# Optimization experiments

Measured on AMD Instinct MI355X. Metric: run time of the kernel, lower is better.

Reference implementation:

```python
import jax, jax.numpy as jnp
import numpy as np

HEADS = 8

def _conv1x1(x, W, b):
    # x: [n, Cin, H, W]; W: [Cout, Cin]; b: [Cout]
    return jnp.einsum('nchw,oc->nohw', x, W) + b[None, :, None, None]

def setup_inputs() -> dict:
    key = jax.random.key(0)
    ks = jax.random.split(key, 11)
    n, Cin, H, W = 8, 256, 80, 80
    Ck, Cv = 256, 256
    s_in = 1.0 / np.sqrt(Cin)
    s_v = 1.0 / np.sqrt(Cv)
    return {
        'query_feature': jax.random.normal(ks[0], (n, Cin, H, W), jnp.float32),
        'key_feature': jax.random.normal(ks[1], (n, Cin, H, W), jnp.float32),
        'value_feature': jax.random.normal(ks[2], (n, Cin, H, W), jnp.float32),
        'Wq': jax.random.normal(ks[3], (Ck, Cin), jnp.float32) * s_in,
        'bq': jax.random.normal(ks[4], (Ck,), jnp.float32) * s_in,
        'Wk': jax.random.normal(ks[5], (Ck, Cin), jnp.float32) * s_in,
        'bk': jax.random.normal(ks[6], (Ck,), jnp.float32) * s_in,
        'Wv': jax.random.normal(ks[7], (Cv, Cin), jnp.float32) * s_in,
        'bv': jax.random.normal(ks[8], (Cv,), jnp.float32) * s_in,
        'Wr': jax.random.normal(ks[9], (Cin, Cv), jnp.float32) * s_v,
        'br': jax.random.normal(ks[10], (Cin,), jnp.float32) * s_v,
    }

def reference(query_feature, key_feature, value_feature, Wq, bq, Wk, bk, Wv, bv, Wr, br):
    n, _, qh, qw = query_feature.shape
    kvn, _, kvh, kvw = key_feature.shape
    Ck = Wq.shape[0]
    Cv = Wv.shape[0]
    hk = Ck // HEADS
    hv = Cv // HEADS
    Lq = qh * qw
    Lkv = kvh * kvw
    # 1x1 conv projections, split channels into heads (consecutive channel blocks)
    q = _conv1x1(query_feature, Wq, bq).reshape(n, HEADS, hk, Lq)
    k = _conv1x1(key_feature, Wk, bk).reshape(kvn, HEADS, hk, Lkv)
    v = _conv1x1(value_feature, Wv, bv).reshape(kvn, HEADS, hv, Lkv)
    # softmax: keys over spatial positions, queries over head channels
    k = jax.nn.softmax(k, axis=3)
    q = jax.nn.softmax(q, axis=2)
    # efficient (linear) attention: context = K @ V^T, out = context^T @ Q
    context = jnp.einsum('nhkl,nhvl->nhkv', k, v)          # [n, H, hk, hv]
    attended = jnp.einsum('nhkv,nhkl->nhvl', context, q)   # [n, H, hv, Lq]
    aggregated = attended.reshape(n, Cv, qh, qw)
    return _conv1x1(aggregated, Wr, br) + query_feature
```

## Files before the change

### kernel.cpp

```cpp
#include <hip/hip_runtime.h>
#include <hip/hip_bf16.h>

#define NB 8
#define C 256
#define LL 6400
#define HEADS 8
#define HC 32
#define NH 64
#define CH 40
#define CHUNK 160
#define KCHUNKS 25

typedef unsigned short u16;
typedef unsigned int u32;
typedef __attribute__((ext_vector_type(8))) short bf16x8;
typedef __attribute__((ext_vector_type(4))) float f32x4;

typedef __attribute__((address_space(1))) const u32 ga_u32;
typedef __attribute__((address_space(3))) u32 ls_u32;

__device__ __forceinline__ void gload_lds16(const u16* g, u16* l) {
  __builtin_amdgcn_global_load_lds((ga_u32*)g, (ls_u32*)l, 16, 0, 0);
}

__device__ __forceinline__ float bf2f(u32 u) { return __uint_as_float(u << 16); }
__device__ __forceinline__ u16 f2bf(float f) {
  __hip_bfloat16 h = __float2bfloat16(f);
  return *(u16*)&h;
}
__device__ __forceinline__ void unpack8(uint4 u, float* f) {
  f[0] = bf2f(u.x & 0xffffu); f[1] = bf2f(u.x >> 16);
  f[2] = bf2f(u.y & 0xffffu); f[3] = bf2f(u.y >> 16);
  f[4] = bf2f(u.z & 0xffffu); f[5] = bf2f(u.z >> 16);
  f[6] = bf2f(u.w & 0xffffu); f[7] = bf2f(u.w >> 16);
}

__global__ __launch_bounds__(256) void transpose_cvt(const float* __restrict__ X,
                                                     u16* __restrict__ Xt) {
  __shared__ float tl[64][65];
  const int n = blockIdx.z, l0 = blockIdx.x * 64, c0 = blockIdx.y * 64;
  const int t = threadIdx.x;
  const int rr = t >> 4;
  const int lc = (t & 15) * 4;
  const float* Xn = X + (size_t)n * C * LL;
#pragma unroll
  for (int p = 0; p < 4; ++p) {
    const int row = p * 16 + rr;
    float4 v = *(const float4*)&Xn[(size_t)(c0 + row) * LL + l0 + lc];
    tl[row][lc + 0] = v.x; tl[row][lc + 1] = v.y;
    tl[row][lc + 2] = v.z; tl[row][lc + 3] = v.w;
  }
  __syncthreads();
  u16* XtN = Xt + (size_t)n * LL * C;
  const int cc = (t & 15) * 4;
#pragma unroll
  for (int p = 0; p < 4; ++p) {
    const int lrow = p * 16 + rr;
    ushort4 o;
    o.x = f2bf(tl[cc + 0][lrow]); o.y = f2bf(tl[cc + 1][lrow]);
    o.z = f2bf(tl[cc + 2][lrow]); o.w = f2bf(tl[cc + 3][lrow]);
    *(ushort4*)&XtN[(size_t)(l0 + lrow) * C + c0 + cc] = o;
  }
}

__global__ __launch_bounds__(256) void cvt_bf16(const float* __restrict__ src,
                                                u16* __restrict__ dst) {
  const int i = (blockIdx.x * 256 + threadIdx.x) * 4;
  float4 v = *(const float4*)&src[i];
  ushort4 o = {f2bf(v.x), f2bf(v.y), f2bf(v.z), f2bf(v.w)};
  *(ushort4*)&dst[i] = o;
}

__global__ __launch_bounds__(256) void proj_mfma(const u16* __restrict__ Xt,
    const u16* __restrict__ Wb, const float* __restrict__ bias,
    u16* __restrict__ Pt) {
  __shared__ __align__(16) u16 As[4096];
  __shared__ __align__(16) u16 Bs[4096];
  const int n = blockIdx.z;
  const int l0 = blockIdx.x * 128;
  const int co0 = blockIdx.y * 128;
  const int t = threadIdx.x;
  const int lane = t & 63, wave = t >> 6;
  const int wm = (wave >> 1) * 64, wn = (wave & 1) * 64;
  const int srow = t >> 2;
  const int scol = (t & 3) * 8;
  const u16* XtN = Xt + (size_t)n * LL * C;
  f32x4 acc[4][4] = {};
  for (int k0 = 0; k0 < C; k0 += 32) {
    __syncthreads();
    gload_lds16(&XtN[(size_t)(l0 + srow) * C + k0 + scol], &As[wave * 512]);
    gload_lds16(&XtN[(size_t)(l0 + 64 + srow) * C + k0 + scol], &As[2048 + wave * 512]);
    gload_lds16(&Wb[(size_t)(co0 + srow) * C + k0 + scol], &Bs[wave * 512]);
    gload_lds16(&Wb[(size_t)(co0 + 64 + srow) * C + k0 + scol], &Bs[2048 + wave * 512]);
    __syncthreads();
    const int fr = lane & 15, quad = lane >> 4;
    bf16x8 a[4], b[4];
#pragma unroll
    for (int i = 0; i < 4; ++i)
      a[i] = *(const bf16x8*)&As[(wm + i * 16 + fr) * 32 + quad * 8];
#pragma unroll
    for (int j = 0; j < 4; ++j)
      b[j] = *(const bf16x8*)&Bs[(wn + j * 16 + fr) * 32 + quad * 8];
#pragma unroll
    for (int i = 0; i < 4; ++i)
#pragma unroll
      for (int j = 0; j < 4; ++j)
        acc[i][j] = __builtin_amdgcn_mfma_f32_16x16x32_bf16(a[i], b[j], acc[i][j], 0, 0, 0);
  }
  u16* PtN = Pt + (size_t)n * LL * C;
  const int fr = lane & 15, quad = lane >> 4;
  const int colc = co0 + wn + fr;
  float bv[4];
#pragma unroll
  for (int j = 0; j < 4; ++j) bv[j] = bias[colc + j * 16];
#pragma unroll
  for (int i = 0; i < 4; ++i) {
    const int lrow = l0 + wm + i * 16 + quad * 4;
#pragma unroll
    for (int r = 0; r < 4; ++r)
#pragma unroll
      for (int j = 0; j < 4; ++j)
        PtN[(size_t)(lrow + r) * C + colc + j * 16] = f2bf(acc[i][j][r] + bv[j]);
  }
}

__global__ __launch_bounds__(256) void kstats(const u16* __restrict__ Kt,
    float* __restrict__ pmax, float* __restrict__ psum) {
  const int chk = blockIdx.x, n = blockIdx.y;
  const int t = threadIdx.x;
  const int c2 = t & 127, ph = t >> 7;
  const u16* base = Kt + ((size_t)n * LL + chk * 256) * C + c2 * 2;
  float m0 = -1e30f, m1 = -1e30f;
  for (int i = 0; i < 128; ++i) {
    u32 u = *(const u32*)&base[(size_t)(2 * i + ph) * C];
    m0 = fmaxf(m0, bf2f(u & 0xffffu)); m1 = fmaxf(m1, bf2f(u >> 16));
  }
  __shared__ float sm[2][256];
  sm[ph][c2 * 2] = m0; sm[ph][c2 * 2 + 1] = m1;
  __syncthreads();
  m0 = fmaxf(sm[0][c2 * 2], sm[1][c2 * 2]);
  m1 = fmaxf(sm[0][c2 * 2 + 1], sm[1][c2 * 2 + 1]);
  float s0 = 0.f, s1 = 0.f;
  for (int i = 0; i < 128; ++i) {
    u32 u = *(const u32*)&base[(size_t)(2 * i + ph) * C];
    s0 += __expf(bf2f(u & 0xffffu) - m0);
    s1 += __expf(bf2f(u >> 16) - m1);
  }
  __syncthreads();
  sm[ph][c2 * 2] = s0; sm[ph][c2 * 2 + 1] = s1;
  __syncthreads();
  if (ph == 0) {
    const int idx = (n * KCHUNKS + chk) * 256 + c2 * 2;
    pmax[idx] = m0; pmax[idx + 1] = m1;
    psum[idx] = sm[0][c2 * 2] + sm[1][c2 * 2];
    psum[idx + 1] = sm[0][c2 * 2 + 1] + sm[1][c2 * 2 + 1];
  }
}

__global__ __launch_bounds__(256) void kmerge(const float* __restrict__ pmax,
    const float* __restrict__ psum, float* __restrict__ kmax, float* __restrict__ krs) {
  const int n = blockIdx.x, c = threadIdx.x;
  float m = -1e30f;
  for (int ch = 0; ch < KCHUNKS; ++ch)
    m = fmaxf(m, pmax[(n * KCHUNKS + ch) * 256 + c]);
  float s = 0.f;
  for (int ch = 0; ch < KCHUNKS; ++ch)
    s += psum[(n * KCHUNKS + ch) * 256 + c] * __expf(pmax[(n * KCHUNKS + ch) * 256 + c] - m);
  kmax[n * 256 + c] = m;
  krs[n * 256 + c] = 1.0f / s;
}

__global__ __launch_bounds__(256) void qsoftmax(u16* __restrict__ Qt) {
  const int t = threadIdx.x;
  const int lane = t & 63, wave = t >> 6;
  const int g = lane >> 2, sub = lane & 3;
  const int gid = (blockIdx.x * 4 + wave) * 16 + g;
  const int h = gid & 7;
  const size_t row = (size_t)(gid >> 3);
  u16* p = Qt + row * C + h * 32 + sub * 8;
  uint4 u = *(const uint4*)p;
  float v[8]; unpack8(u, v);
  float m = v[0];
#pragma unroll
  for (int j = 1; j < 8; ++j) m = fmaxf(m, v[j]);
  m = fmaxf(m, __shfl_xor(m, 1));
  m = fmaxf(m, __shfl_xor(m, 2));
  float e[8], s = 0.f;
#pragma unroll
  for (int j = 0; j < 8; ++j) { e[j] = __expf(v[j] - m); s += e[j]; }
  s += __shfl_xor(s, 1);
  s += __shfl_xor(s, 2);
  const float r = 1.0f / s;
  union { uint4 u; u16 h[8]; } o;
#pragma unroll
  for (int j = 0; j < 8; ++j) o.h[j] = f2bf(e[j] * r);
  *(uint4*)p = o.u;
}

__global__ __launch_bounds__(64) void ctx_partial(const u16* __restrict__ Kt,
    const u16* __restrict__ Vt, const float* __restrict__ kmax,
    const float* __restrict__ krs, float* __restrict__ part) {
  __shared__ float Ks[32][36];
  __shared__ float Vs[32][36];
  const int nh = blockIdx.y, chk = blockIdx.x;
  const int n = nh >> 3, h = nh & 7;
  const int lane = threadIdx.x;
  const int rr = lane >> 2, koff = (lane & 3) * 8;
  float km[8];
#pragma unroll
  for (int j = 0; j < 8; ++j) km[j] = kmax[n * C + h * 32 + koff + j];
  const size_t rowbase = ((size_t)n * LL + chk * CHUNK) * C + h * 32 + koff;
  const int k4 = (lane & 7) * 4, v4 = (lane >> 3) * 4;
  float acc[4][4];
#pragma unroll
  for (int i = 0; i < 4; ++i)
#pragma unroll
    for (int j = 0; j < 4; ++j) acc[i][j] = 0.f;
  for (int ls = 0; ls < CHUNK; ls += 32) {
    __syncthreads();
#pragma unroll
    for (int p = 0; p < 2; ++p) {
      const int r = p * 16 + rr;
      uint4 ku = *(const uint4*)&Kt[rowbase + (size_t)(ls + r) * C];
      uint4 vu = *(const uint4*)&Vt[rowbase + (size_t)(ls + r) * C];
      float kf[8], vf[8];
      unpack8(ku, kf); unpack8(vu, vf);
#pragma unroll
      for (int j = 0; j < 8; ++j) {
        Ks[r][koff + j] = __expf(kf[j] - km[j]);
        Vs[r][koff + j] = vf[j];
      }
    }
    __syncthreads();
#pragma unroll
    for (int l = 0; l < 32; ++l) {
      float a[4], b[4];
      *(float4*)a = *(const float4*)&Ks[l][k4];
      *(float4*)b = *(const float4*)&Vs[l][v4];
#pragma unroll
      for (int i = 0; i < 4; ++i)
#pragma unroll
        for (int j = 0; j < 4; ++j) acc[i][j] = fmaf(a[i], b[j], acc[i][j]);
    }
  }
#pragma unroll
  for (int i = 0; i < 4; ++i) {
    const float rs = krs[n * C + h * 32 + k4 + i];
#pragma unroll
    for (int j = 0; j < 4; ++j)
      part[(((size_t)chk * NH + nh) * HC + k4 + i) * HC + v4 + j] = acc[i][j] * rs;
  }
}

__global__ __launch_bounds__(256) void ctx_reduce(const float* __restrict__ part,
                                                  float* __restrict__ ctx) {
  const int idx = blockIdx.x * 256 + threadIdx.x;
  float s = 0.f;
  for (int c = 0; c < CH; ++c) s += part[(size_t)c * (NH * HC * HC) + idx];
  ctx[idx] = s;
}

__global__ __launch_bounds__(256) void mfuse(const float* __restrict__ Wr,
    const float* __restrict__ ctx, u16* __restrict__ M) {
  const int idx = blockIdx.x * 256 + threadIdx.x;
  const int hk = idx & 255;
  const int o = (idx >> 8) & 255;
  const int n = idx >> 16;
  const int h = hk >> 5, k = hk & 31;
  const float* wr = Wr + (size_t)o * C + h * HC;
  const float* cx = ctx + ((size_t)(n * HEADS + h) * HC + k) * HC;
  float s = 0.f;
#pragma unroll
  for (int v = 0; v < HC; ++v) s = fmaf(wr[v], cx[v], s);
  M[idx] = f2bf(s);
}

__global__ __launch_bounds__(256) void out_mfma(const u16* __restrict__ Qt,
    const u16* __restrict__ Mb, const float* __restrict__ br,
    const float* __restrict__ Xq, float* __restrict__ out) {
  __shared__ __align__(16) u16 As[4096];
  __shared__ __align__(16) u16 Bs[4096];
  const int n = blockIdx.z;
  const int l0 = blockIdx.x * 128;
  const int co0 = blockIdx.y * 128;
  const int t = threadIdx.x;
  const int lane = t & 63, wave = t >> 6;
  const int wm = (wave >> 1) * 64, wn = (wave & 1) * 64;
  const int srow = t >> 2;
  const int scol = (t & 3) * 8;
  const u16* MbN = Mb + (size_t)n * C * C;
  const u16* QtN = Qt + (size_t)n * LL * C;
  f32x4 acc[4][4] = {};
  for (int k0 = 0; k0 < C; k0 += 32) {
    __syncthreads();
    gload_lds16(&MbN[(size_t)(co0 + srow) * C + k0 + scol], &As[wave * 512]);
    gload_lds16(&MbN[(size_t)(co0 + 64 + srow) * C + k0 + scol], &As[2048 + wave * 512]);
    gload_lds16(&QtN[(size_t)(l0 + srow) * C + k0 + scol], &Bs[wave * 512]);
    gload_lds16(&QtN[(size_t)(l0 + 64 + srow) * C + k0 + scol], &Bs[2048 + wave * 512]);
    __syncthreads();
    const int fr = lane & 15, quad = lane >> 4;
    bf16x8 a[4], b[4];
#pragma unroll
    for (int i = 0; i < 4; ++i)
      a[i] = *(const bf16x8*)&As[(wm + i * 16 + fr) * 32 + quad * 8];
#pragma unroll
    for (int j = 0; j < 4; ++j)
      b[j] = *(const bf16x8*)&Bs[(wn + j * 16 + fr) * 32 + quad * 8];
#pragma unroll
    for (int i = 0; i < 4; ++i)
#pragma unroll
      for (int j = 0; j < 4; ++j)
        acc[i][j] = __builtin_amdgcn_mfma_f32_16x16x32_bf16(a[i], b[j], acc[i][j], 0, 0, 0);
  }
  const float* XqN = Xq + (size_t)n * C * LL;
  float* On = out + (size_t)n * C * LL;
  const int fr = lane & 15, quad = lane >> 4;
#pragma unroll
  for (int i = 0; i < 4; ++i) {
#pragma unroll
    for (int r = 0; r < 4; ++r) {
      const int co = co0 + wm + i * 16 + quad * 4 + r;
      const float bb = br[co];
#pragma unroll
      for (int j = 0; j < 4; ++j) {
        const int l = l0 + wn + j * 16 + fr;
        const size_t off = (size_t)co * LL + l;
        On[off] = acc[i][j][r] + bb + XqN[off];
      }
    }
  }
}

extern "C" void kernel_launch(void* const* d_in, const int* in_sizes, int n_in,
                              void* d_out, int out_size, void* d_ws, size_t ws_size,
                              hipStream_t stream) {
  const float* Xq = (const float*)d_in[0];
  const float* Xk = (const float*)d_in[1];
  const float* Xv = (const float*)d_in[2];
  const float* Wq = (const float*)d_in[3];
  const float* bq = (const float*)d_in[4];
  const float* Wk = (const float*)d_in[5];
  const float* bk = (const float*)d_in[6];
  const float* Wv = (const float*)d_in[7];
  const float* bv = (const float*)d_in[8];
  const float* Wr = (const float*)d_in[9];
  const float* br = (const float*)d_in[10];
  float* out = (float*)d_out;

  char* ws = (char*)d_ws;
  const size_t nelem = (size_t)NB * LL * C;
  u16* Xt = (u16*)ws;
  u16* Qt = (u16*)(ws + nelem * 2);
  u16* Kt = (u16*)(ws + nelem * 4);
  u16* Vt = (u16*)(ws + nelem * 6);
  char* p = ws + nelem * 8;
  u16* Wqb = (u16*)p; p += C * C * 2;
  u16* Wkb = (u16*)p; p += C * C * 2;
  u16* Wvb = (u16*)p; p += C * C * 2;
  u16* Mb = (u16*)p;  p += (size_t)NB * C * C * 2;
  float* pmax = (float*)p; p += KCHUNKS * NB * C * 4;
  float* psum = (float*)p; p += KCHUNKS * NB * C * 4;
  float* kmax = (float*)p; p += NB * C * 4;
  float* krs = (float*)p;  p += NB * C * 4;
  float* ctx = (float*)p;  p += NH * HC * HC * 4;
  float* part = (float*)p;

  const dim3 gT(100, 4, NB);
  const dim3 gG(50, 2, NB);

  cvt_bf16<<<64, 256, 0, stream>>>(Wq, Wqb);
  cvt_bf16<<<64, 256, 0, stream>>>(Wk, Wkb);
  cvt_bf16<<<64, 256, 0, stream>>>(Wv, Wvb);

  transpose_cvt<<<gT, 256, 0, stream>>>(Xq, Xt);
  proj_mfma<<<gG, 256, 0, stream>>>(Xt, Wqb, bq, Qt);
  transpose_cvt<<<gT, 256, 0, stream>>>(Xk, Xt);
  proj_mfma<<<gG, 256, 0, stream>>>(Xt, Wkb, bk, Kt);
  transpose_cvt<<<gT, 256, 0, stream>>>(Xv, Xt);
  proj_mfma<<<gG, 256, 0, stream>>>(Xt, Wvb, bv, Vt);

  qsoftmax<<<NB * LL * HEADS / 64, 256, 0, stream>>>(Qt);
  kstats<<<dim3(KCHUNKS, NB), 256, 0, stream>>>(Kt, pmax, psum);
  kmerge<<<NB, 256, 0, stream>>>(pmax, psum, kmax, krs);
  ctx_partial<<<dim3(CH, NH), 64, 0, stream>>>(Kt, Vt, kmax, krs, part);
  ctx_reduce<<<NH * HC * HC / 256, 256, 0, stream>>>(part, ctx);
  mfuse<<<NB * C * C / 256, 256, 0, stream>>>(Wr, ctx, Mb);
  out_mfma<<<gG, 256, 0, stream>>>(Qt, Mb, br, Xq, out);
}
```

Measured before the change: 359.1 us.

## Fuse transpose into projections, drop K max pass, fuse Q softmax into output GEMM

Projections now read fp32 NCHW input directly, converting and transposing into LDS inside a single batched launch for Q, K and V. This removes the bf16 transposed staging buffer and its extra pass. The key softmax no longer computes a running max: exp(k) is accumulated along with its row sums, and normalisation happens in ctx_reduce. The query softmax is computed per tile inside the output GEMM. Removing the max subtraction risks overflow for large key logits.

```diff
diff --git a/kernel.cpp b/kernel.cpp
--- a/kernel.cpp
+++ b/kernel.cpp
@@ -7,9 +7,10 @@
 #define HEADS 8
 #define HC 32
 #define NH 64
-#define CH 40
-#define CHUNK 160
-#define KCHUNKS 25
+#define SEG 40
+#define SL 160
+#define ATP 40
+#define QPP 264
 
 typedef unsigned short u16;
 typedef unsigned int u32;
@@ -35,229 +36,152 @@
   f[6] = bf2f(u.w & 0xffffu); f[7] = bf2f(u.w >> 16);
 }
 
-__global__ __launch_bounds__(256) void transpose_cvt(const float* __restrict__ X,
-                                                     u16* __restrict__ Xt) {
-  __shared__ float tl[64][65];
-  const int n = blockIdx.z, l0 = blockIdx.x * 64, c0 = blockIdx.y * 64;
-  const int t = threadIdx.x;
-  const int rr = t >> 4;
-  const int lc = (t & 15) * 4;
-  const float* Xn = X + (size_t)n * C * LL;
-#pragma unroll
-  for (int p = 0; p < 4; ++p) {
-    const int row = p * 16 + rr;
-    float4 v = *(const float4*)&Xn[(size_t)(c0 + row) * LL + l0 + lc];
-    tl[row][lc + 0] = v.x; tl[row][lc + 1] = v.y;
-    tl[row][lc + 2] = v.z; tl[row][lc + 3] = v.w;
-  }
-  __syncthreads();
-  u16* XtN = Xt + (size_t)n * LL * C;
-  const int cc = (t & 15) * 4;
-#pragma unroll
-  for (int p = 0; p < 4; ++p) {
-    const int lrow = p * 16 + rr;
-    ushort4 o;
-    o.x = f2bf(tl[cc + 0][lrow]); o.y = f2bf(tl[cc + 1][lrow]);
-    o.z = f2bf(tl[cc + 2][lrow]); o.w = f2bf(tl[cc + 3][lrow]);
-    *(ushort4*)&XtN[(size_t)(l0 + lrow) * C + c0 + cc] = o;
-  }
-}
-
-__global__ __launch_bounds__(256) void cvt_bf16(const float* __restrict__ src,
-                                                u16* __restrict__ dst) {
-  const int i = (blockIdx.x * 256 + threadIdx.x) * 4;
-  float4 v = *(const float4*)&src[i];
+struct WcvtArgs { const float* W[3]; u16* Wb[3]; };
+struct PFArgs { const float* X[3]; const u16* Wb[3]; const float* bias[3]; u16* P[3]; };
+
+__global__ __launch_bounds__(256) void wcvt(WcvtArgs a) {
+  const int idx = blockIdx.x * 256 + threadIdx.x;
+  const int which = idx >> 14, off = (idx & 16383) * 4;
+  float4 v = *(const float4*)&a.W[which][off];
   ushort4 o = {f2bf(v.x), f2bf(v.y), f2bf(v.z), f2bf(v.w)};
-  *(ushort4*)&dst[i] = o;
-}
-
-__global__ __launch_bounds__(256) void proj_mfma(const u16* __restrict__ Xt,
-    const u16* __restrict__ Wb, const float* __restrict__ bias,
-    u16* __restrict__ Pt) {
-  __shared__ __align__(16) u16 As[4096];
-  __shared__ __align__(16) u16 Bs[4096];
-  const int n = blockIdx.z;
+  *(ushort4*)&a.Wb[which][off] = o;
+}
+
+__global__ __launch_bounds__(256, 2) void proj_fused(PFArgs args) {
+  __shared__ __align__(16) u16 At[128 * ATP];
+  __shared__ __align__(16) u16 Bs[256 * 32];
+  const int which = blockIdx.y >> 3, n = blockIdx.y & 7;
   const int l0 = blockIdx.x * 128;
-  const int co0 = blockIdx.y * 128;
   const int t = threadIdx.x;
   const int lane = t & 63, wave = t >> 6;
-  const int wm = (wave >> 1) * 64, wn = (wave & 1) * 64;
-  const int srow = t >> 2;
-  const int scol = (t & 3) * 8;
-  const u16* XtN = Xt + (size_t)n * LL * C;
-  f32x4 acc[4][4] = {};
+  const int fr = lane & 15, q = lane >> 4;
+  const int wl = (wave >> 1) * 64, wco = (wave & 1) * 128;
+  const int s32 = t & 31, rcg = t >> 5;
+  const int srow = t >> 2, scol = (t & 3) * 8;
+  const float* X = args.X[which] + (size_t)n * C * LL;
+  const u16* Wb = args.Wb[which];
+  f32x4 acc[4][8] = {};
+  float4 xv[4];
+#pragma unroll
+  for (int j = 0; j < 4; ++j)
+    xv[j] = *(const float4*)&X[(size_t)(rcg * 4 + j) * LL + l0 + s32 * 4];
   for (int k0 = 0; k0 < C; k0 += 32) {
     __syncthreads();
-    gload_lds16(&XtN[(size_t)(l0 + srow) * C + k0 + scol], &As[wave * 512]);
-    gload_lds16(&XtN[(size_t)(l0 + 64 + srow) * C + k0 + scol], &As[2048 + wave * 512]);
-    gload_lds16(&Wb[(size_t)(co0 + srow) * C + k0 + scol], &Bs[wave * 512]);
-    gload_lds16(&Wb[(size_t)(co0 + 64 + srow) * C + k0 + scol], &Bs[2048 + wave * 512]);
+#pragma unroll
+    for (int s = 0; s < 4; ++s)
+      gload_lds16(&Wb[(size_t)(s * 64 + srow) * C + k0 + scol],
+                  &Bs[s * 2048 + wave * 512]);
+    const float* xf = (const float*)xv;
+#pragma unroll
+    for (int li = 0; li < 4; ++li) {
+      const int lp = li ^ (s32 & 3);
+      u32 lo = (u32)f2bf(xf[0 * 4 + lp]) | ((u32)f2bf(xf[1 * 4 + lp]) << 16);
+      u32 hi = (u32)f2bf(xf[2 * 4 + lp]) | ((u32)f2bf(xf[3 * 4 + lp]) << 16);
+      u32* dst = (u32*)&At[(s32 * 4 + lp) * ATP + rcg * 4];
+      dst[0] = lo; dst[1] = hi;
+    }
     __syncthreads();
-    const int fr = lane & 15, quad = lane >> 4;
-    bf16x8 a[4], b[4];
+    if (k0 + 32 < C) {
+#pragma unroll
+      for (int j = 0; j < 4; ++j)
+        xv[j] = *(const float4*)&X[(size_t)(k0 + 32 + rcg * 4 + j) * LL + l0 + s32 * 4];
+    }
+    bf16x8 a[4];
 #pragma unroll
     for (int i = 0; i < 4; ++i)
-      a[i] = *(const bf16x8*)&As[(wm + i * 16 + fr) * 32 + quad * 8];
-#pragma unroll
-    for (int j = 0; j < 4; ++j)
-      b[j] = *(const bf16x8*)&Bs[(wn + j * 16 + fr) * 32 + quad * 8];
+      a[i] = *(const bf16x8*)&At[(wl + i * 16 + fr) * ATP + q * 8];
+#pragma unroll
+    for (int j = 0; j < 8; ++j) {
+      bf16x8 b = *(const bf16x8*)&Bs[(wco + j * 16 + fr) * 32 + q * 8];
+#pragma unroll
+      for (int i = 0; i < 4; ++i)
+        acc[i][j] = __builtin_amdgcn_mfma_f32_16x16x32_bf16(a[i], b, acc[i][j], 0, 0, 0);
+    }
+  }
+  const float* bias = args.bias[which];
+  u16* P = args.P[which] + (size_t)n * LL * C;
+  float bb[8];
+#pragma unroll
+  for (int j = 0; j < 8; ++j) bb[j] = bias[wco + j * 16 + fr];
+#pragma unroll
+  for (int i = 0; i < 4; ++i)
+#pragma unroll
+    for (int r = 0; r < 4; ++r) {
+      const int lrow = l0 + wl + i * 16 + q * 4 + r;
+#pragma unroll
+      for (int j = 0; j < 8; ++j)
+        P[(size_t)lrow * C + wco + j * 16 + fr] = f2bf(acc[i][j][r] + bb[j]);
+    }
+}
+
+__global__ __launch_bounds__(256) void ctx_part(const u16* __restrict__ Kt,
+    const u16* __restrict__ Vt, float* __restrict__ pctx, float* __restrict__ psum) {
+  __shared__ __align__(16) u16 Ks[16 * 256];
+  __shared__ __align__(16) u16 Vs[16 * 256];
+  const int seg = blockIdx.x, n = blockIdx.y;
+  const int t = threadIdx.x, lane = t & 63, wave = t >> 6;
+  const int l0 = seg * SL;
+  const u16* KtN = Kt + (size_t)n * LL * C;
+  const u16* VtN = Vt + (size_t)n * LL * C;
+  const int k4 = (lane & 7) * 4, v8 = lane >> 3;
+  float acc[2][4][4] = {};
+  float ssum[2][4] = {};
+  for (int ls = 0; ls < SL; ls += 16) {
+    __syncthreads();
+#pragma unroll
+    for (int i = 0; i < 2; ++i) {
+      const int r = wave * 4 + i * 2;
+      gload_lds16(&KtN[(size_t)(l0 + ls + r) * C + lane * 8], &Ks[r * 256]);
+      gload_lds16(&VtN[(size_t)(l0 + ls + r) * C + lane * 8], &Vs[r * 256]);
+    }
+    __syncthreads();
+#pragma unroll
+    for (int hh = 0; hh < 2; ++hh) {
+      const int h = wave * 2 + hh;
+#pragma unroll
+      for (int l = 0; l < 16; ++l) {
+        ushort4 ku = *(const ushort4*)&Ks[l * 256 + h * 32 + k4];
+        ushort4 vu = *(const ushort4*)&Vs[l * 256 + h * 32 + v8 * 4];
+        float ek[4] = {__expf(bf2f(ku.x)), __expf(bf2f(ku.y)),
+                       __expf(bf2f(ku.z)), __expf(bf2f(ku.w))};
+        float vf[4] = {bf2f(vu.x), bf2f(vu.y), bf2f(vu.z), bf2f(vu.w)};
+#pragma unroll
+        for (int i = 0; i < 4; ++i)
+#pragma unroll
+          for (int j = 0; j < 4; ++j) acc[hh][i][j] = fmaf(ek[i], vf[j], acc[hh][i][j]);
+        if (v8 == 0)
+#pragma unroll
+          for (int i = 0; i < 4; ++i) ssum[hh][i] += ek[i];
+      }
+    }
+  }
+#pragma unroll
+  for (int hh = 0; hh < 2; ++hh) {
+    const int h = wave * 2 + hh;
+    const size_t pb = ((size_t)seg * NH + n * 8 + h) * 1024;
 #pragma unroll
     for (int i = 0; i < 4; ++i)
 #pragma unroll
       for (int j = 0; j < 4; ++j)
-        acc[i][j] = __builtin_amdgcn_mfma_f32_16x16x32_bf16(a[i], b[j], acc[i][j], 0, 0, 0);
-  }
-  u16* PtN = Pt + (size_t)n * LL * C;
-  const int fr = lane & 15, quad = lane >> 4;
-  const int colc = co0 + wn + fr;
-  float bv[4];
-#pragma unroll
-  for (int j = 0; j < 4; ++j) bv[j] = bias[colc + j * 16];
-#pragma unroll
-  for (int i = 0; i < 4; ++i) {
-    const int lrow = l0 + wm + i * 16 + quad * 4;
-#pragma unroll
-    for (int r = 0; r < 4; ++r)
-#pragma unroll
-      for (int j = 0; j < 4; ++j)
-        PtN[(size_t)(lrow + r) * C + colc + j * 16] = f2bf(acc[i][j][r] + bv[j]);
-  }
-}
-
-__global__ __launch_bounds__(256) void kstats(const u16* __restrict__ Kt,
-    float* __restrict__ pmax, float* __restrict__ psum) {
-  const int chk = blockIdx.x, n = blockIdx.y;
-  const int t = threadIdx.x;
-  const int c2 = t & 127, ph = t >> 7;
-  const u16* base = Kt + ((size_t)n * LL + chk * 256) * C + c2 * 2;
-  float m0 = -1e30f, m1 = -1e30f;
-  for (int i = 0; i < 128; ++i) {
-    u32 u = *(const u32*)&base[(size_t)(2 * i + ph) * C];
-    m0 = fmaxf(m0, bf2f(u & 0xffffu)); m1 = fmaxf(m1, bf2f(u >> 16));
-  }
-  __shared__ float sm[2][256];
-  sm[ph][c2 * 2] = m0; sm[ph][c2 * 2 + 1] = m1;
-  __syncthreads();
-  m0 = fmaxf(sm[0][c2 * 2], sm[1][c2 * 2]);
-  m1 = fmaxf(sm[0][c2 * 2 + 1], sm[1][c2 * 2 + 1]);
-  float s0 = 0.f, s1 = 0.f;
-  for (int i = 0; i < 128; ++i) {
-    u32 u = *(const u32*)&base[(size_t)(2 * i + ph) * C];
-    s0 += __expf(bf2f(u & 0xffffu) - m0);
-    s1 += __expf(bf2f(u >> 16) - m1);
-  }
-  __syncthreads();
-  sm[ph][c2 * 2] = s0; sm[ph][c2 * 2 + 1] = s1;
-  __syncthreads();
-  if (ph == 0) {
-    const int idx = (n * KCHUNKS + chk) * 256 + c2 * 2;
-    pmax[idx] = m0; pmax[idx + 1] = m1;
-    psum[idx] = sm[0][c2 * 2] + sm[1][c2 * 2];
-    psum[idx + 1] = sm[0][c2 * 2 + 1] + sm[1][c2 * 2 + 1];
-  }
-}
-
-__global__ __launch_bounds__(256) void kmerge(const float* __restrict__ pmax,
-    const float* __restrict__ psum, float* __restrict__ kmax, float* __restrict__ krs) {
-  const int n = blockIdx.x, c = threadIdx.x;
-  float m = -1e30f;
-  for (int ch = 0; ch < KCHUNKS; ++ch)
-    m = fmaxf(m, pmax[(n * KCHUNKS + ch) * 256 + c]);
-  float s = 0.f;
-  for (int ch = 0; ch < KCHUNKS; ++ch)
-    s += psum[(n * KCHUNKS + ch) * 256 + c] * __expf(pmax[(n * KCHUNKS + ch) * 256 + c] - m);
-  kmax[n * 256 + c] = m;
-  krs[n * 256 + c] = 1.0f / s;
-}
-
-__global__ __launch_bounds__(256) void qsoftmax(u16* __restrict__ Qt) {
-  const int t = threadIdx.x;
-  const int lane = t & 63, wave = t >> 6;
-  const int g = lane >> 2, sub = lane & 3;
-  const int gid = (blockIdx.x * 4 + wave) * 16 + g;
-  const int h = gid & 7;
-  const size_t row = (size_t)(gid >> 3);
-  u16* p = Qt + row * C + h * 32 + sub * 8;
-  uint4 u = *(const uint4*)p;
-  float v[8]; unpack8(u, v);
-  float m = v[0];
-#pragma unroll
-  for (int j = 1; j < 8; ++j) m = fmaxf(m, v[j]);
-  m = fmaxf(m, __shfl_xor(m, 1));
-  m = fmaxf(m, __shfl_xor(m, 2));
-  float e[8], s = 0.f;
-#pragma unroll
-  for (int j = 0; j < 8; ++j) { e[j] = __expf(v[j] - m); s += e[j]; }
-  s += __shfl_xor(s, 1);
-  s += __shfl_xor(s, 2);
-  const float r = 1.0f / s;
-  union { uint4 u; u16 h[8]; } o;
-#pragma unroll
-  for (int j = 0; j < 8; ++j) o.h[j] = f2bf(e[j] * r);
-  *(uint4*)p = o.u;
-}
-
-__global__ __launch_bounds__(64) void ctx_partial(const u16* __restrict__ Kt,
-    const u16* __restrict__ Vt, const float* __restrict__ kmax,
-    const float* __restrict__ krs, float* __restrict__ part) {
-  __shared__ float Ks[32][36];
-  __shared__ float Vs[32][36];
-  const int nh = blockIdx.y, chk = blockIdx.x;
-  const int n = nh >> 3, h = nh & 7;
-  const int lane = threadIdx.x;
-  const int rr = lane >> 2, koff = (lane & 3) * 8;
-  float km[8];
-#pragma unroll
-  for (int j = 0; j < 8; ++j) km[j] = kmax[n * C + h * 32 + koff + j];
-  const size_t rowbase = ((size_t)n * LL + chk * CHUNK) * C + h * 32 + koff;
-  const int k4 = (lane & 7) * 4, v4 = (lane >> 3) * 4;
-  float acc[4][4];
-#pragma unroll
-  for (int i = 0; i < 4; ++i)
-#pragma unroll
-    for (int j = 0; j < 4; ++j) acc[i][j] = 0.f;
-  for (int ls = 0; ls < CHUNK; ls += 32) {
-    __syncthreads();
-#pragma unroll
-    for (int p = 0; p < 2; ++p) {
-      const int r = p * 16 + rr;
-      uint4 ku = *(const uint4*)&Kt[rowbase + (size_t)(ls + r) * C];
-      uint4 vu = *(const uint4*)&Vt[rowbase + (size_t)(ls + r) * C];
-      float kf[8], vf[8];
-      unpack8(ku, kf); unpack8(vu, vf);
-#pragma unroll
-      for (int j = 0; j < 8; ++j) {
-        Ks[r][koff + j] = __expf(kf[j] - km[j]);
-        Vs[r][koff + j] = vf[j];
-      }
-    }
-    __syncthreads();
-#pragma unroll
-    for (int l = 0; l < 32; ++l) {
-      float a[4], b[4];
-      *(float4*)a = *(const float4*)&Ks[l][k4];
-      *(float4*)b = *(const float4*)&Vs[l][v4];
-#pragma unroll
-      for (int i = 0; i < 4; ++i)
-#pragma unroll
-        for (int j = 0; j < 4; ++j) acc[i][j] = fmaf(a[i], b[j], acc[i][j]);
-    }
-  }
-#pragma unroll
-  for (int i = 0; i < 4; ++i) {
-    const float rs = krs[n * C + h * 32 + k4 + i];
-#pragma unroll
-    for (int j = 0; j < 4; ++j)
-      part[(((size_t)chk * NH + nh) * HC + k4 + i) * HC + v4 + j] = acc[i][j] * rs;
-  }
-}
-
-__global__ __launch_bounds__(256) void ctx_reduce(const float* __restrict__ part,
-                                                  float* __restrict__ ctx) {
+        pctx[pb + (size_t)(k4 + i) * 32 + v8 * 4 + j] = acc[hh][i][j];
+    if (v8 == 0) {
+      const size_t sb = ((size_t)seg * NH + n * 8 + h) * 32;
+#pragma unroll
+      for (int i = 0; i < 4; ++i) psum[sb + k4 + i] = ssum[hh][i];
+    }
+  }
+}
+
+__global__ __launch_bounds__(256) void ctx_reduce(const float* __restrict__ pctx,
+    const float* __restrict__ psum, float* __restrict__ ctx) {
   const int idx = blockIdx.x * 256 + threadIdx.x;
-  float s = 0.f;
-  for (int c = 0; c < CH; ++c) s += part[(size_t)c * (NH * HC * HC) + idx];
-  ctx[idx] = s;
+  const int nh = idx >> 10, e = idx & 1023, k = e >> 5;
+  float s = 0.f, ss = 0.f;
+  for (int g = 0; g < SEG; ++g) {
+    s += pctx[(size_t)(g * NH + nh) * 1024 + e];
+    ss += psum[(size_t)(g * NH + nh) * 32 + k];
+  }
+  ctx[idx] = s / ss;
 }
 
 __global__ __launch_bounds__(256) void mfuse(const float* __restrict__ Wr,
@@ -275,60 +199,78 @@
   M[idx] = f2bf(s);
 }
 
-__global__ __launch_bounds__(256) void out_mfma(const u16* __restrict__ Qt,
+__global__ __launch_bounds__(256) void out_fused(const u16* __restrict__ Qt,
     const u16* __restrict__ Mb, const float* __restrict__ br,
     const float* __restrict__ Xq, float* __restrict__ out) {
-  __shared__ __align__(16) u16 As[4096];
-  __shared__ __align__(16) u16 Bs[4096];
-  const int n = blockIdx.z;
-  const int l0 = blockIdx.x * 128;
-  const int co0 = blockIdx.y * 128;
-  const int t = threadIdx.x;
-  const int lane = t & 63, wave = t >> 6;
-  const int wm = (wave >> 1) * 64, wn = (wave & 1) * 64;
-  const int srow = t >> 2;
-  const int scol = (t & 3) * 8;
+  __shared__ __align__(16) u16 Qp[64 * QPP];
+  __shared__ __align__(16) u16 As[128 * 32];
+  const int n = blockIdx.y, l0 = blockIdx.x * 64;
+  const int t = threadIdx.x, lane = t & 63, wave = t >> 6;
+  const int fr = lane & 15, q = lane >> 4;
+  const int wcoL = (wave >> 1) * 64, wl = (wave & 1) * 32;
+  const u16* QtN = Qt + (size_t)n * LL * C;
+#pragma unroll
+  for (int p = 0; p < 2; ++p) {
+    const int row = p * 32 + (t >> 3);
+    const int g = t & 7;
+    const uint4* src = (const uint4*)&QtN[(size_t)(l0 + row) * C + g * 32];
+    uint4 u0 = src[0], u1 = src[1], u2 = src[2], u3 = src[3];
+    float v[32];
+    unpack8(u0, v); unpack8(u1, v + 8); unpack8(u2, v + 16); unpack8(u3, v + 24);
+    float e[32], s = 0.f;
+#pragma unroll
+    for (int j = 0; j < 32; ++j) { e[j] = __expf(v[j]); s += e[j]; }
+    const float r = 1.0f / s;
+    uint4* drow = (uint4*)&Qp[row * QPP + g * 32];
+#pragma unroll
+    for (int b4 = 0; b4 < 4; ++b4) {
+      union { uint4 u; u16 h[8]; } o;
+#pragma unroll
+      for (int j = 0; j < 8; ++j) o.h[j] = f2bf(e[b4 * 8 + j] * r);
+      drow[b4] = o.u;
+    }
+  }
+  f32x4 acc[2][4][2] = {};
   const u16* MbN = Mb + (size_t)n * C * C;
-  const u16* QtN = Qt + (size_t)n * LL * C;
-  f32x4 acc[4][4] = {};
-  for (int k0 = 0; k0 < C; k0 += 32) {
-    __syncthreads();
-    gload_lds16(&MbN[(size_t)(co0 + srow) * C + k0 + scol], &As[wave * 512]);
-    gload_lds16(&MbN[(size_t)(co0 + 64 + srow) * C + k0 + scol], &As[2048 + wave * 512]);
-    gload_lds16(&QtN[(size_t)(l0 + srow) * C + k0 + scol], &Bs[wave * 512]);
-    gload_lds16(&QtN[(size_t)(l0 + 64 + srow) * C + k0 + scol], &Bs[2048 + wave * 512]);
-    __syncthreads();
-    const int fr = lane & 15, quad = lane >> 4;
-    bf16x8 a[4], b[4];
-#pragma unroll
-    for (int i = 0; i < 4; ++i)
-      a[i] = *(const bf16x8*)&As[(wm + i * 16 + fr) * 32 + quad * 8];
-#pragma unroll
-    for (int j = 0; j < 4; ++j)
-      b[j] = *(const bf16x8*)&Bs[(wn + j * 16 + fr) * 32 + quad * 8];
-#pragma unroll
-    for (int i = 0; i < 4; ++i)
-#pragma unroll
-      for (int j = 0; j < 4; ++j)
-        acc[i][j] = __builtin_amdgcn_mfma_f32_16x16x32_bf16(a[i], b[j], acc[i][j], 0, 0, 0);
-  }
+  const int srow = t >> 2, scol = (t & 3) * 8;
+  for (int coh = 0; coh < 2; ++coh)
+    for (int k0 = 0; k0 < C; k0 += 32) {
+      __syncthreads();
+#pragma unroll
+      for (int s = 0; s < 2; ++s)
+        gload_lds16(&MbN[(size_t)(coh * 128 + s * 64 + srow) * C + k0 + scol],
+                    &As[s * 2048 + wave * 512]);
+      __syncthreads();
+      bf16x8 a[4], b[2];
+#pragma unroll
+      for (int i = 0; i < 4; ++i)
+        a[i] = *(const bf16x8*)&As[(wcoL + i * 16 + fr) * 32 + q * 8];
+#pragma unroll
+      for (int j = 0; j < 2; ++j)
+        b[j] = *(const bf16x8*)&Qp[(wl + j * 16 + fr) * QPP + k0 + q * 8];
+#pragma unroll
+      for (int i = 0; i < 4; ++i)
+#pragma unroll
+        for (int j = 0; j < 2; ++j)
+          acc[coh][i][j] = __builtin_amdgcn_mfma_f32_16x16x32_bf16(a[i], b[j], acc[coh][i][j], 0, 0, 0);
+    }
   const float* XqN = Xq + (size_t)n * C * LL;
   float* On = out + (size_t)n * C * LL;
-  const int fr = lane & 15, quad = lane >> 4;
-#pragma unroll
-  for (int i = 0; i < 4; ++i) {
-#pragma unroll
-    for (int r = 0; r < 4; ++r) {
-      const int co = co0 + wm + i * 16 + quad * 4 + r;
-      const float bb = br[co];
-#pragma unroll
-      for (int j = 0; j < 4; ++j) {
-        const int l = l0 + wn + j * 16 + fr;
-        const size_t off = (size_t)co * LL + l;
-        On[off] = acc[i][j][r] + bb + XqN[off];
+#pragma unroll
+  for (int coh = 0; coh < 2; ++coh)
+#pragma unroll
+    for (int i = 0; i < 4; ++i)
+#pragma unroll
+      for (int r = 0; r < 4; ++r) {
+        const int co = coh * 128 + wcoL + i * 16 + q * 4 + r;
+        const float bb = br[co];
+#pragma unroll
+        for (int j = 0; j < 2; ++j) {
+          const int l = l0 + wl + j * 16 + fr;
+          const size_t off = (size_t)co * LL + l;
+          On[off] = acc[coh][i][j][r] + bb + XqN[off];
+        }
       }
-    }
-  }
 }
 
 extern "C" void kernel_launch(void* const* d_in, const int* in_sizes, int n_in,
@@ -349,41 +291,32 @@
 
   char* ws = (char*)d_ws;
   const size_t nelem = (size_t)NB * LL * C;
-  u16* Xt = (u16*)ws;
-  u16* Qt = (u16*)(ws + nelem * 2);
-  u16* Kt = (u16*)(ws + nelem * 4);
-  u16* Vt = (u16*)(ws + nelem * 6);
-  char* p = ws + nelem * 8;
+  u16* Qt = (u16*)ws;
+  u16* Kt = (u16*)(ws + nelem * 2);
+  u16* Vt = (u16*)(ws + nelem * 4);
+  char* p = ws + nelem * 6;
   u16* Wqb = (u16*)p; p += C * C * 2;
   u16* Wkb = (u16*)p; p += C * C * 2;
   u16* Wvb = (u16*)p; p += C * C * 2;
-  u16* Mb = (u16*)p;  p += (size_t)NB * C * C * 2;
-  float* pmax = (float*)p; p += KCHUNKS * NB * C * 4;
-  float* psum = (float*)p; p += KCHUNKS * NB * C * 4;
-  float* kmax = (float*)p; p += NB * C * 4;
-  float* krs = (float*)p;  p += NB * C * 4;
-  float* ctx = (float*)p;  p += NH * HC * HC * 4;
-  float* part = (float*)p;
-
-  const dim3 gT(100, 4, NB);
-  const dim3 gG(50, 2, NB);
-
-  cvt_bf16<<<64, 256, 0, stream>>>(Wq, Wqb);
-  cvt_bf16<<<64, 256, 0, stream>>>(Wk, Wkb);
-  cvt_bf16<<<64, 256, 0, stream>>>(Wv, Wvb);
-
-  transpose_cvt<<<gT, 256, 0, stream>>>(Xq, Xt);
-  proj_mfma<<<gG, 256, 0, stream>>>(Xt, Wqb, bq, Qt);
-  transpose_cvt<<<gT, 256, 0, stream>>>(Xk, Xt);
-  proj_mfma<<<gG, 256, 0, stream>>>(Xt, Wkb, bk, Kt);
-  transpose_cvt<<<gT, 256, 0, stream>>>(Xv, Xt);
-  proj_mfma<<<gG, 256, 0, stream>>>(Xt, Wvb, bv, Vt);
-
-  qsoftmax<<<NB * LL * HEADS / 64, 256, 0, stream>>>(Qt);
-  kstats<<<dim3(KCHUNKS, NB), 256, 0, stream>>>(Kt, pmax, psum);
-  kmerge<<<NB, 256, 0, stream>>>(pmax, psum, kmax, krs);
-  ctx_partial<<<dim3(CH, NH), 64, 0, stream>>>(Kt, Vt, kmax, krs, part);
-  ctx_reduce<<<NH * HC * HC / 256, 256, 0, stream>>>(part, ctx);
+  float* pctx = (float*)p; p += (size_t)SEG * NH * HC * HC * 4;
+  float* psum = (float*)p; p += (size_t)SEG * NH * HC * 4;
+  float* ctx = (float*)p;  p += (size_t)NH * HC * HC * 4;
+  u16* Mb = (u16*)p;
+
+  WcvtArgs wa;
+  wa.W[0] = Wq; wa.W[1] = Wk; wa.W[2] = Wv;
+  wa.Wb[0] = Wqb; wa.Wb[1] = Wkb; wa.Wb[2] = Wvb;
+  wcvt<<<192, 256, 0, stream>>>(wa);
+
+  PFArgs pa;
+  pa.X[0] = Xq; pa.X[1] = Xk; pa.X[2] = Xv;
+  pa.Wb[0] = Wqb; pa.Wb[1] = Wkb; pa.Wb[2] = Wvb;
+  pa.bias[0] = bq; pa.bias[1] = bk; pa.bias[2] = bv;
+  pa.P[0] = Qt; pa.P[1] = Kt; pa.P[2] = Vt;
+  proj_fused<<<dim3(50, 24), 256, 0, stream>>>(pa);
+
+  ctx_part<<<dim3(SEG, NB), 256, 0, stream>>>(Kt, Vt, pctx, psum);
+  ctx_reduce<<<NH * HC * HC / 256, 256, 0, stream>>>(pctx, psum, ctx);
   mfuse<<<NB * C * C / 256, 256, 0, stream>>>(Wr, ctx, Mb);
-  out_mfma<<<gG, 256, 0, stream>>>(Qt, Mb, br, Xq, out);
-}
+  out_fused<<<dim3(100, NB), 256, 0, stream>>>(Qt, Mb, br, Xq, out);
+}
```

New measurement: 347.7 us. 1.03x faster.
